# Kernel optimization log

Hardware: AMD Instinct MI355X
Metric: run time of the kernel (lower is better)

## Reference

```python
import jax, jax.numpy as jnp
import numpy as np

DIN, HID = 256, 512
SCALE = 1.0 / (64.0 * 6.0 ** 2)  # q / 2304, as in the torch code
NEG = 9e15


def setup_inputs() -> dict:
    key = jax.random.key(0)
    ks = jax.random.split(key, 8)
    B, N = 32, 1024
    x = jax.random.normal(ks[0], (B, N, DIN), dtype=jnp.float32)
    mask = jax.random.randint(ks[1], (B, N, N), 0, 2).astype(jnp.float32)
    lim = 1.0 / np.sqrt(DIN)
    Wv = jax.random.uniform(ks[2], (DIN, HID), minval=-lim, maxval=lim, dtype=jnp.float32)
    bv = jax.random.uniform(ks[3], (HID,), minval=-lim, maxval=lim, dtype=jnp.float32)
    Wk = jax.random.uniform(ks[4], (DIN, HID), minval=-lim, maxval=lim, dtype=jnp.float32)
    bk = jax.random.uniform(ks[5], (HID,), minval=-lim, maxval=lim, dtype=jnp.float32)
    Wq = jax.random.uniform(ks[6], (DIN, HID), minval=-lim, maxval=lim, dtype=jnp.float32)
    bq = jax.random.uniform(ks[7], (HID,), minval=-lim, maxval=lim, dtype=jnp.float32)
    return {"x": x, "mask": mask, "Wv": Wv, "bv": bv, "Wk": Wk, "bk": bk, "Wq": Wq, "bq": bq}


def reference(x, mask, Wv, bv, Wk, bk, Wq, bq):
    v = jax.nn.relu(x @ Wv + bv)                      # [B,N,H]
    q = jax.nn.relu(x @ Wq + bq)                      # [B,N,H]
    k = jax.nn.relu(x @ Wk + bk)                      # [B,N,H]
    scores = jnp.einsum('bnh,bmh->bnm', q * SCALE, k)  # [B,N,N]
    att = jax.nn.softmax(scores * mask - NEG * (1.0 - mask), axis=2)
    out = jax.nn.relu(jnp.einsum('bnm,bmh->bnh', att, v))
    return out
```

## Files before the change

### kernel.cpp

```cpp
#include <hip/hip_runtime.h>
#include <hip/hip_bf16.h>

#define DIN   256
#define HID   512
#define NBAT  32
#define NSEQ  1024
#define SCALEF (1.0f / 2304.0f)
#define NEGC  9e15f

typedef __attribute__((ext_vector_type(4))) float f32x4;
typedef __attribute__((ext_vector_type(8))) short bf16x8;
typedef unsigned short u16;

__device__ __forceinline__ u16 f2bf(float f) {
    union { float f; unsigned u; } v; v.f = f;
    unsigned r = v.u + 0x7fffu + ((v.u >> 16) & 1u);
    return (u16)(r >> 16);
}

__device__ __forceinline__ float bf2f(u16 b) {
    union { unsigned u; float f; } v; v.u = ((unsigned)b) << 16;
    return v.f;
}

__device__ __forceinline__ void g2lds16(const void* g, void* l) {
    __builtin_amdgcn_global_load_lds(
        (const __attribute__((address_space(1))) void*)g,
        (__attribute__((address_space(3))) void*)l,
        16, 0, 0);
}

__global__ __launch_bounds__(256) void prep_x(const float* __restrict__ x,
                                              u16* __restrict__ xb) {
    long i = (long)blockIdx.x * 256 + threadIdx.x;
    const long n4 = (long)NBAT * NSEQ * DIN / 4;
    if (i < n4) {
        float4 v = ((const float4*)x)[i];
        ushort4 o;
        o.x = f2bf(v.x); o.y = f2bf(v.y); o.z = f2bf(v.z); o.w = f2bf(v.w);
        ((ushort4*)xb)[i] = o;
    }
}

__global__ __launch_bounds__(256) void prep_w(
    const float* __restrict__ Wv, const float* __restrict__ bv,
    const float* __restrict__ Wk, const float* __restrict__ bk,
    const float* __restrict__ Wq, const float* __restrict__ bq,
    u16* __restrict__ Wtb, float* __restrict__ biascat) {
    int i = blockIdx.x * 256 + threadIdx.x;
    if (i < 1536 * 256) {
        int n = i >> 8, k = i & 255;
        const float* W = (n < 512) ? Wv : ((n < 1024) ? Wk : Wq);
        Wtb[i] = f2bf(W[k * 512 + (n & 511)]);
    }
    if (i < 1536) {
        biascat[i] = (i < 512) ? bv[i] : ((i < 1024) ? bk[i - 512] : bq[i - 1024]);
    }
}

template<int EPI, int BM, int SWZ>
__global__ __launch_bounds__(256) void gemm_t(
    const u16* __restrict__ A, int lda, long sA,
    const u16* __restrict__ Bt, int ldb, long sB,
    void* __restrict__ Cv, int ldc, long sC,
    int K, const float* __restrict__ bias, int gx, int gy) {
    __shared__ u16 lA[BM * 32];
    __shared__ u16 lB[128 * 32];
    const int t = threadIdx.x;
    const int lane = t & 63;
    const int w = t >> 6;

    int b, bxi, byi;
    if (SWZ) {
        int f = (int)blockIdx.x;
        int per = gx * gy;
        int j = f >> 3;
        b = (f & 7) + 8 * (j / per);
        int r = j % per;
        bxi = r % gx; byi = r / gx;
    } else {
        b = blockIdx.z; bxi = blockIdx.x; byi = blockIdx.y;
    }

    const u16* Ab = A + (long)b * sA;
    const u16* Bb = Bt + (long)b * sB;
    const int bm = bxi * BM, bn = byi * 128;

    const int srow = t >> 2;
    const int soff = (t & 3) * 8;
    const u16* gA0 = Ab + (long)(bm + srow) * lda + soff;
    const u16* gA1 = Ab + (long)(bm + srow + 64) * lda + soff;
    const u16* gB0 = Bb + (long)(bn + srow) * ldb + soff;
    const u16* gB1 = Bb + (long)(bn + srow + 64) * ldb + soff;

    constexpr int NJ = (BM == 128) ? 4 : 2;
    const int wr = (BM == 128) ? (w >> 1) * 64 : 0;
    const int wc = (BM == 128) ? (w & 1) * 64 : w * 32;
    const int frow = lane & 15, fk = (lane >> 4) * 8;

    f32x4 acc[4][NJ] = {};

    for (int k0 = 0; k0 < K; k0 += 32) {
        __syncthreads();
        g2lds16(gA0 + k0, &lA[t * 8]);
        if (BM == 128) g2lds16(gA1 + k0, &lA[2048 + t * 8]);
        g2lds16(gB0 + k0, &lB[t * 8]);
        g2lds16(gB1 + k0, &lB[2048 + t * 8]);
        __syncthreads();

        bf16x8 af[4], bfr[NJ];
#pragma unroll
        for (int i = 0; i < 4; ++i)
            af[i] = *(const bf16x8*)&lA[(wr + i * 16 + frow) * 32 + fk];
#pragma unroll
        for (int j = 0; j < NJ; ++j)
            bfr[j] = *(const bf16x8*)&lB[(wc + j * 16 + frow) * 32 + fk];
#pragma unroll
        for (int i = 0; i < 4; ++i)
#pragma unroll
            for (int j = 0; j < NJ; ++j)
                acc[i][j] = __builtin_amdgcn_mfma_f32_16x16x32_bf16(
                    af[i], bfr[j], acc[i][j], 0, 0, 0);
    }

    const int crow0 = bm + wr + (lane >> 4) * 4;
    const int ccol0 = bn + wc + (lane & 15);
#pragma unroll
    for (int i = 0; i < 4; ++i) {
#pragma unroll
        for (int j = 0; j < NJ; ++j) {
            int col = ccol0 + j * 16;
#pragma unroll
            for (int r = 0; r < 4; ++r) {
                int row = crow0 + i * 16 + r;
                float v = acc[i][j][r];
                if (EPI == 0) {
                    v += bias[col];
                    v = v > 0.0f ? v : 0.0f;
                    if (col >= 1024) v *= SCALEF;
                    ((u16*)Cv)[(long)b * sC + (long)row * ldc + col] = f2bf(v);
                } else if (EPI == 1) {
                    ((u16*)Cv)[(long)b * sC + (long)row * ldc + col] = f2bf(v);
                } else {
                    ((float*)Cv)[(long)b * sC + (long)row * ldc + col] =
                        v > 0.0f ? v : 0.0f;
                }
            }
        }
    }
}

__global__ __launch_bounds__(256) void transpose_v(const u16* __restrict__ qkv,
                                                   u16* __restrict__ vt) {
    __shared__ u16 tile[64][72];
    const int t = threadIdx.x;
    const int b = blockIdx.z;
    const int n0 = blockIdx.x * 64, h0 = blockIdx.y * 64;
    const u16* src = qkv + (long)(b * NSEQ + n0) * 1536 + h0;
#pragma unroll
    for (int it = 0; it < 2; ++it) {
        int n = (t >> 3) + it * 32;
        int hc = (t & 7) * 8;
        *(bf16x8*)&tile[n][hc] = *(const bf16x8*)&src[(long)n * 1536 + hc];
    }
    __syncthreads();
    u16* dst = vt + ((long)b * HID + h0) * NSEQ + n0;
#pragma unroll
    for (int it = 0; it < 2; ++it) {
        int h = (t >> 3) + it * 32;
        int nc = (t & 7) * 8;
        bf16x8 v;
#pragma unroll
        for (int j = 0; j < 8; ++j) v[j] = (short)tile[nc + j][h];
        *(bf16x8*)&dst[(long)h * NSEQ + nc] = v;
    }
}

__global__ __launch_bounds__(256) void softmax_mask(
    u16* __restrict__ SP, const float* __restrict__ mask) {
    const long row = blockIdx.x;
    const int t = threadIdx.x;
    ushort4 sv = ((const ushort4*)(SP + row * NSEQ))[t];
    float4 mv = ((const float4*)(mask + row * NSEQ))[t];
    float l0 = mv.x * bf2f(sv.x) - NEGC * (1.0f - mv.x);
    float l1 = mv.y * bf2f(sv.y) - NEGC * (1.0f - mv.y);
    float l2 = mv.z * bf2f(sv.z) - NEGC * (1.0f - mv.z);
    float l3 = mv.w * bf2f(sv.w) - NEGC * (1.0f - mv.w);

    float mx = fmaxf(fmaxf(l0, l1), fmaxf(l2, l3));
#pragma unroll
    for (int off = 32; off; off >>= 1) mx = fmaxf(mx, __shfl_xor(mx, off));
    __shared__ float redm[4];
    if ((t & 63) == 0) redm[t >> 6] = mx;
    __syncthreads();
    mx = fmaxf(fmaxf(redm[0], redm[1]), fmaxf(redm[2], redm[3]));

    float e0 = __expf(l0 - mx), e1 = __expf(l1 - mx);
    float e2 = __expf(l2 - mx), e3 = __expf(l3 - mx);
    float sum = (e0 + e1) + (e2 + e3);
#pragma unroll
    for (int off = 32; off; off >>= 1) sum += __shfl_xor(sum, off);
    __shared__ float reds[4];
    if ((t & 63) == 0) reds[t >> 6] = sum;
    __syncthreads();
    sum = (reds[0] + reds[1]) + (reds[2] + reds[3]);

    float inv = 1.0f / sum;
    ushort4 o;
    o.x = f2bf(e0 * inv); o.y = f2bf(e1 * inv);
    o.z = f2bf(e2 * inv); o.w = f2bf(e3 * inv);
    ((ushort4*)(SP + row * NSEQ))[t] = o;
}

extern "C" void kernel_launch(void* const* d_in, const int* in_sizes, int n_in,
                              void* d_out, int out_size, void* d_ws, size_t ws_size,
                              hipStream_t stream) {
    const float* x    = (const float*)d_in[0];
    const float* mask = (const float*)d_in[1];
    const float* Wv   = (const float*)d_in[2];
    const float* bv   = (const float*)d_in[3];
    const float* Wk   = (const float*)d_in[4];
    const float* bk   = (const float*)d_in[5];
    const float* Wq   = (const float*)d_in[6];
    const float* bq   = (const float*)d_in[7];
    float* out = (float*)d_out;

    char* ws = (char*)d_ws;
    u16*   xb      = (u16*)ws;   ws += (long)NBAT * NSEQ * DIN * 2;
    u16*   Wtb     = (u16*)ws;   ws += (long)1536 * 256 * 2;
    float* biascat = (float*)ws; ws += 1536 * 4;
    u16*   qkv     = (u16*)ws;   ws += (long)NBAT * NSEQ * 1536 * 2;
    u16*   vt      = (u16*)ws;   ws += (long)NBAT * HID * NSEQ * 2;
    u16*   SP      = (u16*)ws;   ws += (long)NBAT * NSEQ * NSEQ * 2;

    prep_x<<<8192, 256, 0, stream>>>(x, xb);
    prep_w<<<1536, 256, 0, stream>>>(Wv, bv, Wk, bk, Wq, bq, Wtb, biascat);

    gemm_t<0, 128, 0><<<dim3(256, 12, 1), 256, 0, stream>>>(
        xb, 256, 0L, Wtb, 256, 0L, qkv, 1536, 0L, 256, biascat, 0, 0);

    transpose_v<<<dim3(16, 8, NBAT), 256, 0, stream>>>(qkv, vt);

    const long sQKV = (long)NSEQ * 1536;
    gemm_t<1, 128, 1><<<NBAT * 8 * 8, 256, 0, stream>>>(
        qkv + 1024, 1536, sQKV, qkv + 512, 1536, sQKV,
        SP, NSEQ, (long)NSEQ * NSEQ, 512, nullptr, 8, 8);

    softmax_mask<<<NBAT * NSEQ, 256, 0, stream>>>(SP, mask);

    gemm_t<2, 64, 1><<<NBAT * 16 * 4, 256, 0, stream>>>(
        SP, NSEQ, (long)NSEQ * NSEQ, vt, NSEQ, (long)HID * NSEQ,
        out, HID, (long)NSEQ * HID, NSEQ, nullptr, 16, 4);
}
```

Before: 426.5 us.

## Use 128x128x64 GEMM tiles with XOR-swizzled LDS layout for all GEMMs

Result: faster. 411.1 us (-3.6%).

```diff
diff --git a/kernel.cpp b/kernel.cpp
--- a/kernel.cpp
+++ b/kernel.cpp
@@ -58,14 +58,14 @@
     }
 }
 
-template<int EPI, int BM, int SWZ>
+template<int EPI, int SWZ>
 __global__ __launch_bounds__(256) void gemm_t(
     const u16* __restrict__ A, int lda, long sA,
     const u16* __restrict__ Bt, int ldb, long sB,
     void* __restrict__ Cv, int ldc, long sC,
     int K, const float* __restrict__ bias, int gx, int gy) {
-    __shared__ u16 lA[BM * 32];
-    __shared__ u16 lB[128 * 32];
+    __shared__ u16 lA[128 * 64];
+    __shared__ u16 lB[128 * 64];
     const int t = threadIdx.x;
     const int lane = t & 63;
     const int w = t >> 6;
@@ -84,43 +84,45 @@
 
     const u16* Ab = A + (long)b * sA;
     const u16* Bb = Bt + (long)b * sB;
-    const int bm = bxi * BM, bn = byi * 128;
-
-    const int srow = t >> 2;
-    const int soff = (t & 3) * 8;
-    const u16* gA0 = Ab + (long)(bm + srow) * lda + soff;
-    const u16* gA1 = Ab + (long)(bm + srow + 64) * lda + soff;
-    const u16* gB0 = Bb + (long)(bn + srow) * ldb + soff;
-    const u16* gB1 = Bb + (long)(bn + srow + 64) * ldb + soff;
-
-    constexpr int NJ = (BM == 128) ? 4 : 2;
-    const int wr = (BM == 128) ? (w >> 1) * 64 : 0;
-    const int wc = (BM == 128) ? (w & 1) * 64 : w * 32;
-    const int frow = lane & 15, fk = (lane >> 4) * 8;
-
-    f32x4 acc[4][NJ] = {};
-
-    for (int k0 = 0; k0 < K; k0 += 32) {
+    const int bm = bxi * 128, bn = byi * 128;
+
+    const int srow = t >> 3;
+    const int csrc = ((t & 7) ^ (srow & 7)) * 8;
+    const u16* gA0 = Ab + (long)(bm + srow) * lda + csrc;
+    const u16* gB0 = Bb + (long)(bn + srow) * ldb + csrc;
+
+    const int wr = (w >> 1) * 64, wc = (w & 1) * 64;
+    const int frow = lane & 15;
+    const int kq = lane >> 4;
+
+    f32x4 acc[4][4] = {};
+
+    for (int k0 = 0; k0 < K; k0 += 64) {
         __syncthreads();
-        g2lds16(gA0 + k0, &lA[t * 8]);
-        if (BM == 128) g2lds16(gA1 + k0, &lA[2048 + t * 8]);
-        g2lds16(gB0 + k0, &lB[t * 8]);
-        g2lds16(gB1 + k0, &lB[2048 + t * 8]);
+#pragma unroll
+        for (int p = 0; p < 4; ++p) {
+            g2lds16(gA0 + (long)p * 32 * lda + k0, &lA[p * 2048 + t * 8]);
+            g2lds16(gB0 + (long)p * 32 * ldb + k0, &lB[p * 2048 + t * 8]);
+        }
         __syncthreads();
 
-        bf16x8 af[4], bfr[NJ];
-#pragma unroll
-        for (int i = 0; i < 4; ++i)
-            af[i] = *(const bf16x8*)&lA[(wr + i * 16 + frow) * 32 + fk];
-#pragma unroll
-        for (int j = 0; j < NJ; ++j)
-            bfr[j] = *(const bf16x8*)&lB[(wc + j * 16 + frow) * 32 + fk];
-#pragma unroll
-        for (int i = 0; i < 4; ++i)
-#pragma unroll
-            for (int j = 0; j < NJ; ++j)
-                acc[i][j] = __builtin_amdgcn_mfma_f32_16x16x32_bf16(
-                    af[i], bfr[j], acc[i][j], 0, 0, 0);
+#pragma unroll
+        for (int kk = 0; kk < 2; ++kk) {
+            const int sc = ((kk * 4 + kq) ^ (frow & 7)) * 8;
+            bf16x8 af[4], bfr[4];
+#pragma unroll
+            for (int i = 0; i < 4; ++i)
+                af[i] = *(const bf16x8*)&lA[(wr + i * 16 + frow) * 64 + sc];
+#pragma unroll
+            for (int j = 0; j < 4; ++j)
+                bfr[j] = *(const bf16x8*)&lB[(wc + j * 16 + frow) * 64 + sc];
+#pragma unroll
+            for (int i = 0; i < 4; ++i)
+#pragma unroll
+                for (int j = 0; j < 4; ++j)
+                    acc[i][j] = __builtin_amdgcn_mfma_f32_16x16x32_bf16(
+                        af[i], bfr[j], acc[i][j], 0, 0, 0);
+        }
     }
 
     const int crow0 = bm + wr + (lane >> 4) * 4;
@@ -128,7 +130,7 @@
 #pragma unroll
     for (int i = 0; i < 4; ++i) {
 #pragma unroll
-        for (int j = 0; j < NJ; ++j) {
+        for (int j = 0; j < 4; ++j) {
             int col = ccol0 + j * 16;
 #pragma unroll
             for (int r = 0; r < 4; ++r) {
@@ -236,19 +238,19 @@
     prep_x<<<8192, 256, 0, stream>>>(x, xb);
     prep_w<<<1536, 256, 0, stream>>>(Wv, bv, Wk, bk, Wq, bq, Wtb, biascat);
 
-    gemm_t<0, 128, 0><<<dim3(256, 12, 1), 256, 0, stream>>>(
+    gemm_t<0, 0><<<dim3(256, 12, 1), 256, 0, stream>>>(
         xb, 256, 0L, Wtb, 256, 0L, qkv, 1536, 0L, 256, biascat, 0, 0);
 
     transpose_v<<<dim3(16, 8, NBAT), 256, 0, stream>>>(qkv, vt);
 
     const long sQKV = (long)NSEQ * 1536;
-    gemm_t<1, 128, 1><<<NBAT * 8 * 8, 256, 0, stream>>>(
+    gemm_t<1, 1><<<NBAT * 8 * 8, 256, 0, stream>>>(
         qkv + 1024, 1536, sQKV, qkv + 512, 1536, sQKV,
         SP, NSEQ, (long)NSEQ * NSEQ, 512, nullptr, 8, 8);
 
     softmax_mask<<<NBAT * NSEQ, 256, 0, stream>>>(SP, mask);
 
-    gemm_t<2, 64, 1><<<NBAT * 16 * 4, 256, 0, stream>>>(
+    gemm_t<2, 1><<<NBAT * 8 * 4, 256, 0, stream>>>(
         SP, NSEQ, (long)NSEQ * NSEQ, vt, NSEQ, (long)HID * NSEQ,
-        out, HID, (long)NSEQ * HID, NSEQ, nullptr, 16, 4);
-}
+        out, HID, (long)NSEQ * HID, NSEQ, nullptr, 8, 4);
+}
```
